# Kernel tuning notes

Hardware: AMD Instinct MI355X
Metric: run time of the kernel (lower is better)

Reference implementation:

```python
import jax, jax.numpy as jnp
import numpy as np

N1, N2, D = 8192, 8192, 128

def setup_inputs() -> dict:
    key = jax.random.key(0)
    k1, k2 = jax.random.split(key)
    desc1 = jax.random.normal(k1, (N1, D), dtype=jnp.float32)
    desc2 = jax.random.normal(k2, (N2, D), dtype=jnp.float32)
    return {"desc1": desc1, "desc2": desc2}

def reference(desc1, desc2):
    # sim: [N1, N2] descriptor similarity matrix
    sim = desc1 @ desc2.T
    # mutual nearest-neighbor matching ('nnm' mode)
    nn12 = jnp.argmax(sim, axis=1)            # [N1] best match in image 2 for each kp in image 1
    nn21 = jnp.argmax(sim, axis=0)            # [N2] best match in image 1 for each kp in image 2
    ids1 = jnp.arange(sim.shape[0])
    mutual = nn21[nn12] == ids1               # mutual-consistency check
    # dense jit-friendly encoding of the ragged match list: -1 where no mutual match
    matches0 = jnp.where(mutual, nn12, -1)    # [N1] int
    # matching_scores0 = top-1 similarity per row (torch.topk(..., k=1)[0].squeeze())
    scores = jnp.max(sim, axis=1)             # [N1]
    return matches0, scores
```

## Files before the change

### kernel.cpp

```cpp
#include <hip/hip_runtime.h>
#include <stdint.h>

#define N1 8192
#define N2 8192
#define DK 128
#define TAU 0.08f
#define BIAS 256.0f
#define LDR 132

typedef _Float16 half8 __attribute__((ext_vector_type(8)));
typedef _Float16 half4 __attribute__((ext_vector_type(4)));
typedef float floatx4 __attribute__((ext_vector_type(4)));

__device__ __align__(16) _Float16 g_Af[N1 * DK];
__device__ __align__(16) _Float16 g_Bf[N2 * DK];
__device__ __align__(16) float2 g_rowtop2[64 * N1];
__device__ __align__(16) float2 g_coltop2[64 * N2];
__device__ int g_nn12[N1];
__device__ int g_nn21[N2];

__device__ __forceinline__ float bval(float key) {
    return __uint_as_float(__float_as_uint(key) & 0xFFFFFF80u);
}
__device__ __forceinline__ int bidx(float key) {
    return (int)(__float_as_uint(key) & 127u);
}
__device__ __forceinline__ void push2f(float& t1, float& t2, float p) {
    float m = __builtin_amdgcn_fmed3f(t1, t2, p);
    t1 = fmaxf(t1, p);
    t2 = m;
}
__device__ __forceinline__ void merge2f(float& t1, float& t2, float o1, float o2) {
    float x = fmaxf(t2, o2);
    float m = __builtin_amdgcn_fmed3f(t1, o1, x);
    t1 = fmaxf(t1, o1);
    t2 = m;
}
__device__ __forceinline__ float2 m2(float2 a, float2 b) {
    merge2f(a.x, a.y, b.x, b.y);
    return a;
}
#define DPPF(x, ctrl) __int_as_float(__builtin_amdgcn_update_dpp( \
        0, __float_as_int(x), (ctrl), 0xF, 0xF, true))

__device__ __forceinline__ unsigned mono32(float v) {
    unsigned u = __float_as_uint(v);
    return u ^ ((u & 0x80000000u) ? 0xFFFFFFFFu : 0x80000000u);
}
__device__ __forceinline__ float unmono32(unsigned k) {
    unsigned u = (k & 0x80000000u) ? (k ^ 0x80000000u) : ~k;
    return __uint_as_float(u);
}
__device__ __forceinline__ unsigned long long pack64(float d, unsigned idx) {
    return ((unsigned long long)mono32(d) << 32) | (unsigned)(~idx);
}

__global__ __launch_bounds__(256) void convert_kernel(const float* __restrict__ A,
                                                      const float* __restrict__ B) {
    int t = blockIdx.x * blockDim.x + threadIdx.x;
    const int perMat = N1 * (DK / 4);
    int which = (t >= perMat) ? 1 : 0;
    const float* src = which ? B : A;
    _Float16* dst = which ? g_Bf : g_Af;
    int i = which ? t - perMat : t;
    int m = i >> 5;
    int kq = i & 31;
    float4 v = *reinterpret_cast<const float4*>(src + (size_t)m * DK + kq * 4);
    half4 h = {(_Float16)v.x, (_Float16)v.y, (_Float16)v.z, (_Float16)v.w};
    *reinterpret_cast<half4*>(dst + (size_t)m * DK + kq * 4) = h;
}

__global__ __launch_bounds__(256) void simf16_kernel() {
    __shared__ union {
        _Float16 Bs[128 * LDR];
        float2 scr[128][34];
    } sm;
    __shared__ float2 lmerge[2][128];

    const int tid  = threadIdx.x;
    const int lane = tid & 63;
    const int wave = tid >> 6;
    const int wm = wave >> 1, wn = wave & 1;
    const int fr = lane & 15, q = lane >> 4;

    const int flat = blockIdx.y * 64 + blockIdx.x;
    const int xcd = flat & 7;
    const int j = flat >> 3;
    const int ty = j >> 3;
    const int tx = ((j & 7) << 3) | xcd;
    const int row0 = ty * 128, col0 = tx * 128;

#pragma unroll
    for (int i = 0; i < 8; ++i) {
        int f = i * 256 + tid;
        int r = f >> 4, c = f & 15;
        *reinterpret_cast<float4*>(&sm.Bs[r * LDR + c * 8]) =
            *reinterpret_cast<const float4*>(g_Bf + (size_t)(col0 + r) * DK + c * 8);
    }

    floatx4 acc[4][4];
#pragma unroll
    for (int mt = 0; mt < 4; ++mt)
#pragma unroll
        for (int nt = 0; nt < 4; ++nt)
            acc[mt][nt] = (floatx4){0.f, 0.f, 0.f, 0.f};

    const _Float16* Abase = g_Af + (size_t)(row0 + wm * 64 + fr) * DK + q * 8;

    half8 af[4], afn[4];
#pragma unroll
    for (int mt = 0; mt < 4; ++mt)
        af[mt] = *reinterpret_cast<const half8*>(Abase + mt * 16 * DK);

    __syncthreads();

#pragma unroll
    for (int ks = 0; ks < 4; ++ks) {
        if (ks < 3) {
#pragma unroll
            for (int mt = 0; mt < 4; ++mt)
                afn[mt] = *reinterpret_cast<const half8*>(Abase + mt * 16 * DK + (ks + 1) * 32);
        }
        half8 bf[4];
#pragma unroll
        for (int nt = 0; nt < 4; ++nt)
            bf[nt] = *reinterpret_cast<const half8*>(&sm.Bs[(wn * 64 + nt * 16 + fr) * LDR + ks * 32 + q * 8]);
        __builtin_amdgcn_s_setprio(1);
#pragma unroll
        for (int mt = 0; mt < 4; ++mt)
#pragma unroll
            for (int nt = 0; nt < 4; ++nt)
                acc[mt][nt] = __builtin_amdgcn_mfma_f32_16x16x32_f16(af[mt], bf[nt], acc[mt][nt], 0, 0, 0);
        __builtin_amdgcn_s_setprio(0);
        if (ks < 3) {
#pragma unroll
            for (int mt = 0; mt < 4; ++mt)
                af[mt] = afn[mt];
        }
    }

    __syncthreads();

#pragma unroll
    for (int mt = 0; mt < 4; ++mt)
#pragma unroll
        for (int nt = 0; nt < 4; ++nt)
#pragma unroll
            for (int reg = 0; reg < 4; ++reg)
                acc[mt][nt][reg] = __uint_as_float(
                    __float_as_uint(acc[mt][nt][reg] + BIAS) & 0xFFFFFF80u);

#pragma unroll
    for (int mt = 0; mt < 4; ++mt) {
#pragma unroll
        for (int reg = 0; reg < 4; ++reg) {
            float t1 = 0.f, t2 = 0.f;
#pragma unroll
            for (int nt = 0; nt < 4; ++nt)
                push2f(t1, t2, __uint_as_float(__float_as_uint(acc[mt][nt][reg])
                                               | (unsigned)(wn * 64 + nt * 16 + fr)));
            sm.scr[wm * 64 + mt * 16 + q * 4 + reg][wn * 16 + fr] = make_float2(t1, t2);
        }
    }
    __syncthreads();

    {
        const int row = tid >> 1, h = tid & 1;
        const float4* p = reinterpret_cast<const float4*>(&sm.scr[row][h * 16]);
        float4 v0 = p[0], v1 = p[1], v2 = p[2], v3 = p[3];
        float4 v4 = p[4], v5 = p[5], v6 = p[6], v7 = p[7];
        float2 r0 = m2(make_float2(v0.x, v0.y), make_float2(v0.z, v0.w));
        float2 r1 = m2(make_float2(v1.x, v1.y), make_float2(v1.z, v1.w));
        float2 r2 = m2(make_float2(v2.x, v2.y), make_float2(v2.z, v2.w));
        float2 r3 = m2(make_float2(v3.x, v3.y), make_float2(v3.z, v3.w));
        float2 r4 = m2(make_float2(v4.x, v4.y), make_float2(v4.z, v4.w));
        float2 r5 = m2(make_float2(v5.x, v5.y), make_float2(v5.z, v5.w));
        float2 r6 = m2(make_float2(v6.x, v6.y), make_float2(v6.z, v6.w));
        float2 r7 = m2(make_float2(v7.x, v7.y), make_float2(v7.z, v7.w));
        r0 = m2(r0, r1); r2 = m2(r2, r3); r4 = m2(r4, r5); r6 = m2(r6, r7);
        r0 = m2(r0, r2); r4 = m2(r4, r6);
        r0 = m2(r0, r4);
        float o1 = __shfl_xor(r0.x, 1, 64), o2 = __shfl_xor(r0.y, 1, 64);
        merge2f(r0.x, r0.y, o1, o2);
        if (h == 0) g_rowtop2[(size_t)tx * N1 + row0 + row] = r0;
    }

#pragma unroll
    for (int nt = 0; nt < 4; ++nt) {
        float t1 = 0.f, t2 = 0.f;
#pragma unroll
        for (int mt = 0; mt < 4; ++mt)
#pragma unroll
            for (int reg = 0; reg < 4; ++reg)
                push2f(t1, t2, __uint_as_float(__float_as_uint(acc[mt][nt][reg])
                                               | (unsigned)(wm * 64 + mt * 16 + q * 4 + reg)));
        float o1 = __shfl_xor(t1, 16, 64), o2 = __shfl_xor(t2, 16, 64);
        merge2f(t1, t2, o1, o2);
        o1 = __shfl_xor(t1, 32, 64); o2 = __shfl_xor(t2, 32, 64);
        merge2f(t1, t2, o1, o2);
        if (q == 0) lmerge[wm][wn * 64 + nt * 16 + fr] = make_float2(t1, t2);
    }
    __syncthreads();
    if (tid < 128) {
        float2 a = lmerge[0][tid], b = lmerge[1][tid];
        merge2f(a.x, a.y, b.x, b.y);
        g_coltop2[(size_t)ty * N2 + col0 + tid] = a;
    }
}

__global__ __launch_bounds__(256) void fix_kernel(const float* __restrict__ A,
                                                  const float* __restrict__ B,
                                                  float* __restrict__ out) {
    __shared__ float2 tile[64 * 16];
    __shared__ unsigned long long slot[16];
    __shared__ int cand[256];
    __shared__ int cand_cnt;

    const int tid = threadIdx.x;
    const bool rowside = blockIdx.x >= 512;
    const int base0 = (blockIdx.x & 511) * 16;
    const float2* top2 = rowside ? g_rowtop2 : g_coltop2;

#pragma unroll
    for (int i = 0; i < 4; ++i) {
        int idx = i * 256 + tid;
        int grp = idx >> 4, c = idx & 15;
        tile[grp * 16 + c] = top2[(size_t)grp * N1 + base0 + c];
    }
    if (tid < 16) slot[tid] = 0ULL;
    if (tid == 0) cand_cnt = 0;
    __syncthreads();

    const int c = tid >> 4, j = tid & 15;
    float mx = 0.f;
#pragma unroll
    for (int s = 0; s < 4; ++s)
        mx = fmaxf(mx, tile[(j * 4 + s) * 16 + c].x);
    mx = fmaxf(mx, DPPF(mx, 0xB1));
    mx = fmaxf(mx, DPPF(mx, 0x4E));
    mx = fmaxf(mx, DPPF(mx, 0x124));
    mx = fmaxf(mx, DPPF(mx, 0x128));
    const float thr = bval(mx) - TAU;
#pragma unroll
    for (int s = 0; s < 4; ++s) {
        int grp = j * 4 + s;
        float2 e = tile[grp * 16 + c];
        if (bval(e.x) >= thr) {
            int o = grp * 128 + bidx(e.x);
            int si = atomicAdd(&cand_cnt, 1);
            if (si < 256) cand[si] = (c << 16) | o;
        }
        if (bval(e.y) >= thr) {
            int o = grp * 128 + bidx(e.y);
            int si = atomicAdd(&cand_cnt, 1);
            if (si < 256) cand[si] = (c << 16) | o;
        }
    }
    __syncthreads();

    const int nc = min(cand_cnt, 256);
    for (int i = tid; i < nc; i += 256) {
        int pc = cand[i];
        int cl = pc >> 16, other = pc & 0xFFFF;
        const float* ar = rowside ? (A + (size_t)(base0 + cl) * DK) : (A + (size_t)other * DK);
        const float* br = rowside ? (B + (size_t)other * DK) : (B + (size_t)(base0 + cl) * DK);
        float d = 0.0f;
#pragma unroll
        for (int k4 = 0; k4 < DK / 4; ++k4) {
            float4 a = *reinterpret_cast<const float4*>(ar + k4 * 4);
            float4 b = *reinterpret_cast<const float4*>(br + k4 * 4);
            d = fmaf(a.x, b.x, d);
            d = fmaf(a.y, b.y, d);
            d = fmaf(a.z, b.z, d);
            d = fmaf(a.w, b.w, d);
        }
        atomicMax(&slot[cl], pack64(d, (unsigned)other));
    }
    __syncthreads();

    if (tid < 16) {
        unsigned long long p = slot[tid];
        int idx = base0 + tid;
        if (rowside) {
            g_nn12[idx] = (int)(~(unsigned)p);
            out[N1 + idx] = unmono32((unsigned)(p >> 32));
        } else {
            g_nn21[idx] = (int)(~(unsigned)p);
        }
    }
}

__global__ __launch_bounds__(256) void mutual_kernel(float* __restrict__ out) {
    int i = blockIdx.x * blockDim.x + threadIdx.x;
    if (i < N1) {
        int m = g_nn12[i];
        out[i] = (float)((g_nn21[m] == i) ? m : -1);
    }
}

extern "C" void kernel_launch(void* const* d_in, const int* in_sizes, int n_in,
                              void* d_out, int out_size, void* d_ws, size_t ws_size,
                              hipStream_t stream) {
    const float* A = (const float*)d_in[0];
    const float* B = (const float*)d_in[1];
    float* out = (float*)d_out;

    convert_kernel<<<2 * N1 * (DK / 4) / 256, 256, 0, stream>>>(A, B);
    dim3 grid(64, 64);
    simf16_kernel<<<grid, 256, 0, stream>>>();
    fix_kernel<<<1024, 256, 0, stream>>>(A, B, out);
    mutual_kernel<<<N1 / 256, 256, 0, stream>>>(out);
}
```

Baseline: 116.5 us.

## Fold mutual check into fix kernel via global counter; reorder sim epilogue

Removes the separate mutual_kernel launch. Column-side blocks of fix_kernel publish nn21 and bump a global counter, while row-side blocks spin until all 512 column blocks are done and then perform the mutual check directly. The sim kernel epilogue is also reordered so the column top-2 reduction runs before the first barrier, which drops one __syncthreads. The spin-wait assumes the column blocks (lower block indices) get scheduled before or alongside the waiting row blocks. It also relies on relaxed atomics without an explicit fence, which carries a small ordering risk.

Result: no change. 118.4 us (+1.6%).

```diff
diff --git a/kernel.cpp b/kernel.cpp
--- a/kernel.cpp
+++ b/kernel.cpp
@@ -16,8 +16,8 @@
 __device__ __align__(16) _Float16 g_Bf[N2 * DK];
 __device__ __align__(16) float2 g_rowtop2[64 * N1];
 __device__ __align__(16) float2 g_coltop2[64 * N2];
-__device__ int g_nn12[N1];
 __device__ int g_nn21[N2];
+__device__ int g_col_done;
 
 __device__ __forceinline__ float bval(float key) {
     return __uint_as_float(__float_as_uint(key) & 0xFFFFFF80u);
@@ -57,6 +57,7 @@
 
 __global__ __launch_bounds__(256) void convert_kernel(const float* __restrict__ A,
                                                       const float* __restrict__ B) {
+    if (blockIdx.x == 0 && threadIdx.x == 0) g_col_done = 0;
     int t = blockIdx.x * blockDim.x + threadIdx.x;
     const int perMat = N1 * (DK / 4);
     int which = (t >= perMat) ? 1 : 0;
@@ -139,8 +140,6 @@
         }
     }
 
-    __syncthreads();
-
 #pragma unroll
     for (int mt = 0; mt < 4; ++mt)
 #pragma unroll
@@ -149,6 +148,24 @@
             for (int reg = 0; reg < 4; ++reg)
                 acc[mt][nt][reg] = __uint_as_float(
                     __float_as_uint(acc[mt][nt][reg] + BIAS) & 0xFFFFFF80u);
+
+#pragma unroll
+    for (int nt = 0; nt < 4; ++nt) {
+        float t1 = 0.f, t2 = 0.f;
+#pragma unroll
+        for (int mt = 0; mt < 4; ++mt)
+#pragma unroll
+            for (int reg = 0; reg < 4; ++reg)
+                push2f(t1, t2, __uint_as_float(__float_as_uint(acc[mt][nt][reg])
+                                               | (unsigned)(wm * 64 + mt * 16 + q * 4 + reg)));
+        float o1 = __shfl_xor(t1, 16, 64), o2 = __shfl_xor(t2, 16, 64);
+        merge2f(t1, t2, o1, o2);
+        o1 = __shfl_xor(t1, 32, 64); o2 = __shfl_xor(t2, 32, 64);
+        merge2f(t1, t2, o1, o2);
+        if (q == 0) lmerge[wm][wn * 64 + nt * 16 + fr] = make_float2(t1, t2);
+    }
+
+    __syncthreads();
 
 #pragma unroll
     for (int mt = 0; mt < 4; ++mt) {
@@ -161,6 +178,12 @@
                                                | (unsigned)(wn * 64 + nt * 16 + fr)));
             sm.scr[wm * 64 + mt * 16 + q * 4 + reg][wn * 16 + fr] = make_float2(t1, t2);
         }
+    }
+
+    if (tid < 128) {
+        float2 a = lmerge[0][tid], b = lmerge[1][tid];
+        merge2f(a.x, a.y, b.x, b.y);
+        g_coltop2[(size_t)ty * N2 + col0 + tid] = a;
     }
     __syncthreads();
 
@@ -184,28 +207,6 @@
         merge2f(r0.x, r0.y, o1, o2);
         if (h == 0) g_rowtop2[(size_t)tx * N1 + row0 + row] = r0;
     }
-
-#pragma unroll
-    for (int nt = 0; nt < 4; ++nt) {
-        float t1 = 0.f, t2 = 0.f;
-#pragma unroll
-        for (int mt = 0; mt < 4; ++mt)
-#pragma unroll
-            for (int reg = 0; reg < 4; ++reg)
-                push2f(t1, t2, __uint_as_float(__float_as_uint(acc[mt][nt][reg])
-                                               | (unsigned)(wm * 64 + mt * 16 + q * 4 + reg)));
-        float o1 = __shfl_xor(t1, 16, 64), o2 = __shfl_xor(t2, 16, 64);
-        merge2f(t1, t2, o1, o2);
-        o1 = __shfl_xor(t1, 32, 64); o2 = __shfl_xor(t2, 32, 64);
-        merge2f(t1, t2, o1, o2);
-        if (q == 0) lmerge[wm][wn * 64 + nt * 16 + fr] = make_float2(t1, t2);
-    }
-    __syncthreads();
-    if (tid < 128) {
-        float2 a = lmerge[0][tid], b = lmerge[1][tid];
-        merge2f(a.x, a.y, b.x, b.y);
-        g_coltop2[(size_t)ty * N2 + col0 + tid] = a;
-    }
 }
 
 __global__ __launch_bounds__(256) void fix_kernel(const float* __restrict__ A,
@@ -278,23 +279,35 @@
     }
     __syncthreads();
 
-    if (tid < 16) {
-        unsigned long long p = slot[tid];
-        int idx = base0 + tid;
-        if (rowside) {
-            g_nn12[idx] = (int)(~(unsigned)p);
-            out[N1 + idx] = unmono32((unsigned)(p >> 32));
-        } else {
-            g_nn21[idx] = (int)(~(unsigned)p);
-        }
-    }
-}
-
-__global__ __launch_bounds__(256) void mutual_kernel(float* __restrict__ out) {
-    int i = blockIdx.x * blockDim.x + threadIdx.x;
-    if (i < N1) {
-        int m = g_nn12[i];
-        out[i] = (float)((g_nn21[m] == i) ? m : -1);
+    if (!rowside) {
+        if (tid < 16) {
+            unsigned long long p = slot[tid];
+            __hip_atomic_store(&g_nn21[base0 + tid], (int)(~(unsigned)p),
+                               __ATOMIC_RELAXED, __HIP_MEMORY_SCOPE_AGENT);
+        }
+        __syncthreads();
+        if (tid == 0)
+            __hip_atomic_fetch_add(&g_col_done, 1,
+                                   __ATOMIC_RELAXED, __HIP_MEMORY_SCOPE_AGENT);
+    } else {
+        int m_local = 0;
+        if (tid < 16) {
+            unsigned long long p = slot[tid];
+            m_local = (int)(~(unsigned)p);
+            out[N1 + base0 + tid] = unmono32((unsigned)(p >> 32));
+        }
+        if (tid == 0) {
+            while (__hip_atomic_load(&g_col_done, __ATOMIC_RELAXED,
+                                     __HIP_MEMORY_SCOPE_AGENT) < 512)
+                __builtin_amdgcn_s_sleep(8);
+        }
+        __syncthreads();
+        if (tid < 16) {
+            int v21 = __hip_atomic_load(&g_nn21[m_local], __ATOMIC_RELAXED,
+                                        __HIP_MEMORY_SCOPE_AGENT);
+            int idx = base0 + tid;
+            out[idx] = (float)((v21 == idx) ? m_local : -1);
+        }
     }
 }
 
@@ -309,5 +322,4 @@
     dim3 grid(64, 64);
     simf16_kernel<<<grid, 256, 0, stream>>>();
     fix_kernel<<<1024, 256, 0, stream>>>(A, B, out);
-    mutual_kernel<<<N1 / 256, 256, 0, stream>>>(out);
-}
+}
```
